# Optimization experiments

Hardware: AMD Instinct MI355X
Metric: run time of the kernel (lower is better)

Reference implementation:

```python
import jax, jax.numpy as jnp
import numpy as np

E = 32  # embedding_dim
B = 1048576

def setup_inputs() -> dict:
    key = jax.random.key(0)
    ks = jax.random.split(key, 16)
    def p(k, shape, scale=0.1):
        return jax.random.normal(k, shape, dtype=jnp.float32) * scale
    return {
        'x': jax.random.normal(ks[0], (B, 2, 5), dtype=jnp.float32),
        'fc_emb_w': p(ks[1], (E, 5)), 'fc_emb_b': p(ks[2], (E,)),
        'in_proj_w': p(ks[3], (3 * E, E)), 'in_proj_b': p(ks[4], (3 * E,)),
        'out_proj_w': p(ks[5], (E, E)), 'out_proj_b': p(ks[6], (E,)),
        'w_ih': p(ks[7], (E, E)), 'b_ih': p(ks[8], (E,)),
        'w_hh': p(ks[9], (E, E)), 'b_hh': p(ks[10], (E,)),
        'fc_dec_w': p(ks[11], (5, E)), 'fc_dec_b': p(ks[12], (5,)),
        'out_w': p(ks[13], (3, 5)), 'out_b': p(ks[14], (3,)),
    }

def gelu(x):
    return jax.nn.gelu(x, approximate=False)  # torch nn.GELU default (erf)

def reference(x, fc_emb_w, fc_emb_b, in_proj_w, in_proj_b,
              out_proj_w, out_proj_b, w_ih, b_ih, w_hh, b_hh,
              fc_dec_w, fc_dec_b, out_w, out_b):
    # per-token embedding: [B,2,5] -> [B,2,E]
    e = gelu(jnp.einsum('bsi,ei->bse', x, fc_emb_w) + fc_emb_b)
    # single-head self-attention (seq_len=2)
    wq, wk, wv = jnp.split(in_proj_w, 3, axis=0)
    bq, bk, bv = jnp.split(in_proj_b, 3, axis=0)
    q = jnp.einsum('bsd,ed->bse', e, wq) + bq
    k = jnp.einsum('bsd,ed->bse', e, wk) + bk
    v = jnp.einsum('bsd,ed->bse', e, wv) + bv
    scores = jnp.einsum('bqd,bkd->bqk', q, k) / jnp.sqrt(jnp.float32(E))
    attn = jax.nn.softmax(scores, axis=-1)
    o = jnp.einsum('bqk,bkd->bqd', attn, v)
    o = jnp.einsum('bsd,ed->bse', o, out_proj_w) + out_proj_b
    # 2-step tanh RNN, h0 = 0; final hidden state only
    h1 = jnp.tanh(o[:, 0] @ w_ih.T + b_ih + b_hh)
    h2 = jnp.tanh(o[:, 1] @ w_ih.T + b_ih + h1 @ w_hh.T + b_hh)
    # decode
    d = gelu(h2 @ fc_dec_w.T + fc_dec_b)
    return d @ out_w.T + out_b  # [B,3]
```

## Files before the change

kernel.cpp:

```cpp
#include <hip/hip_runtime.h>
#include <math.h>

#define BT 256

typedef _Float16 half2v __attribute__((ext_vector_type(2)));
typedef __fp16   fp16x2 __attribute__((ext_vector_type(2)));
typedef _Float16 half8  __attribute__((ext_vector_type(8)));
typedef float    f32x16 __attribute__((ext_vector_type(16)));

union U4H8 { unsigned int u[4]; half8 h; };

__device__ __forceinline__ half2v u2h(unsigned int u){
  union { unsigned int u; half2v h; } c; c.u = u; return c.h;
}
__device__ __forceinline__ unsigned int h2u(half2v h){
  union { unsigned int u; half2v h; } c; c.h = h; return c.u;
}
__device__ __forceinline__ half2v pkrtz(float a, float b){
  union { fp16x2 f; half2v h; } c;
  c.f = __builtin_amdgcn_cvt_pkrtz(a, b);
  return c.h;
}
__device__ __forceinline__ float fdot2(half2v a, half2v b, float c){
  return __builtin_amdgcn_fdot2(a, b, c, false);
}
__device__ __forceinline__ float frcp(float x){ return __builtin_amdgcn_rcpf(x); }

__device__ __forceinline__ unsigned int pk_rne(float a, float b){
  half2v h; h.x = (_Float16)a; h.y = (_Float16)b; return h2u(h);
}

__device__ __forceinline__ float gelu_erf(float v){
  float z  = v * 0.70710678118654752f;
  float az = fabsf(z);
  float t  = frcp(fmaf(0.47047f, az, 1.0f));
  float poly = t*fmaf(t, fmaf(t, 0.7478556f, -0.0958798f), 0.3480242f);
  float ex = __expf(-az*az);
  float erfv = fmaf(-poly, ex, 1.0f);
  erfv = (z < 0.0f) ? -erfv : erfv;
  return 0.5f*v*(1.0f + erfv);
}
__device__ __forceinline__ float tanh_fast(float v){
  float t = __expf(2.0f*v);
  return 1.0f - 2.0f*frcp(t + 1.0f);
}

__device__ __forceinline__ half2v gelu_pk(half2v x){
  const _Float16 a0 = (_Float16)0.3989423f,  a1 = (_Float16)-0.0663157f,
                 a2 = (_Float16)0.0096298f,  a3 = (_Float16)-0.00095967f,
                 a4 = (_Float16)0.000048f,   hp = (_Float16)0.5f,
                 hn = (_Float16)-0.5f;
  const half2v A0={a0,a0}, A1={a1,a1}, A2={a2,a2}, A3={a3,a3}, A4={a4,a4};
  const half2v HP={hp,hp}, HN={hn,hn};
  half2v t = x*x;
  half2v q = A4*t + A3;
  q = q*t + A2;
  q = q*t + A1;
  q = q*t + A0;
  half2v u = x*q;
#if __has_builtin(__builtin_elementwise_min)
  u = __builtin_elementwise_max(u, HN);
  u = __builtin_elementwise_min(u, HP);
#else
  u.x = u.x > hp ? hp : (u.x < hn ? hn : u.x);
  u.y = u.y > hp ? hp : (u.y < hn ? hn : u.y);
#endif
  return x*(u + HP);
}

__global__ void prep_kernel(const float* __restrict__ inw, const float* __restrict__ inb,
                            const float* __restrict__ opw, const float* __restrict__ opb,
                            const float* __restrict__ wih, const float* __restrict__ bih,
                            const float* __restrict__ bhh, const float* __restrict__ whh,
                            const float* __restrict__ decw, const float* __restrict__ embw,
                            const float* __restrict__ decb,
                            unsigned int* __restrict__ wsu){
  __shared__ float sA[1024], sP[1024], sM[1024], sT[32], sWV[32], sBM[32];
  int tx = threadIdx.x & 31;
  int ty = threadIdx.x >> 5;
  float accA = 0.f, accP = 0.f;
  #pragma unroll
  for (int m = 0; m < 32; m++){
    accA += inw[m*32 + ty] * inw[1024 + m*32 + tx];
    accP += opw[ty*32 + m] * inw[2048 + m*32 + tx];
  }
  sA[ty*32 + tx] = accA;
  sP[ty*32 + tx] = accP;
  if (ty == 0){
    float aw = 0.f;
    #pragma unroll
    for (int m = 0; m < 32; m++) aw += inb[m] * inw[1024 + m*32 + tx];
    sWV[tx] = aw;
  }
  if (ty == 1){
    float at = opb[tx];
    #pragma unroll
    for (int m = 0; m < 32; m++) at += opw[tx*32 + m] * inb[64 + m];
    sT[tx] = at;
  }
  __syncthreads();
  float accM = 0.f;
  #pragma unroll
  for (int m = 0; m < 32; m++) accM += wih[ty*32 + m] * sP[m*32 + tx];
  sM[ty*32 + tx] = accM;
  if (ty == 2){
    float ab = bih[tx] + bhh[tx];
    #pragma unroll
    for (int m = 0; m < 32; m++) ab += wih[tx*32 + m] * sT[m];
    sBM[tx] = ab;
  }
  __syncthreads();
  int t = threadIdx.x;
  if (t < 512){
    int r = t >> 4, c2 = (t & 15)*2;
    wsu[t]        = pk_rne(sA[r*32+c2],  sA[r*32+c2+1]);
    wsu[512 + t]  = pk_rne(sM[r*32+c2],  sM[r*32+c2+1]);
    wsu[1024 + t] = pk_rne(whh[r*32+c2], whh[r*32+c2+1]);
    wsu[1536 + t] = (r < 5) ? pk_rne(decw[r*32+c2], decw[r*32+c2+1]) : 0u;
  } else {
    int q = t - 512;
    if (q < 256){
      int j = q >> 3, cc = (q & 7)*2;
      float a = (cc   < 5) ? embw[j*5+cc]   : 0.f;
      float b = (cc+1 < 5) ? embw[j*5+cc+1] : 0.f;
      wsu[2048 + q] = pk_rne(a, b);
    } else if (q < 272){
      int k = (q - 256)*2;
      wsu[2304 + (q-256)] = pk_rne(sWV[k], sWV[k+1]);
    } else if (q < 304){
      ((float*)wsu)[2320 + (q-272)] = sBM[q-272];
    } else if (q < 336){
      int i = q - 304;
      ((float*)wsu)[2352 + i] = (i < 5) ? decb[i] : 0.f;
    }
  }
}

__device__ __forceinline__ half8 ldfrag(const unsigned int* __restrict__ p){
  U4H8 t; t.u[0]=p[0]; t.u[1]=p[1]; t.u[2]=p[2]; t.u[3]=p[3]; return t.h;
}

struct BF { U4H8 b1, b2; };
__device__ __forceinline__ BF toB_pk(const unsigned int* pk, bool g){
  unsigned int s0 = g?pk[0]:pk[2], s1 = g?pk[1]:pk[3],
               s2 = g?pk[4]:pk[6], s3 = g?pk[5]:pk[7];
  unsigned int r0 = __shfl_xor(s0,32), r1 = __shfl_xor(s1,32);
  unsigned int r2 = __shfl_xor(s2,32), r3 = __shfl_xor(s3,32);
  BF o;
  o.b1.u[0]=g?r0:pk[0]; o.b1.u[1]=g?r1:pk[1]; o.b1.u[2]=g?pk[2]:r0; o.b1.u[3]=g?pk[3]:r1;
  o.b2.u[0]=g?r2:pk[4]; o.b2.u[1]=g?r3:pk[5]; o.b2.u[2]=g?pk[6]:r2; o.b2.u[3]=g?pk[7]:r3;
  return o;
}

__device__ __forceinline__ f32x16 ldbias(const float* __restrict__ p, int grp){
  const float4* b = (const float4*)(p + 4*grp);
  float4 q0 = b[0], q1 = b[2], q2 = b[4], q3 = b[6];
  f32x16 c;
  c[0]=q0.x; c[1]=q0.y; c[2]=q0.z; c[3]=q0.w;
  c[4]=q1.x; c[5]=q1.y; c[6]=q1.z; c[7]=q1.w;
  c[8]=q2.x; c[9]=q2.y; c[10]=q2.z; c[11]=q2.w;
  c[12]=q3.x; c[13]=q3.y; c[14]=q3.z; c[15]=q3.w;
  return c;
}

__global__ __launch_bounds__(BT) void fused_kernel(
    const float* __restrict__ x,
    const unsigned int* __restrict__ wsu,
    const float* __restrict__ embb,
    const float* __restrict__ outw, const float* __restrict__ outb,
    float* __restrict__ y, int B)
{
  int tid  = threadIdx.x;
  int lane = tid & 63;
  int col  = lane & 31;
  bool g   = (lane >> 5) != 0;
  int grp  = g ? 1 : 0;
  long long base = ((long long)blockIdx.x*(BT/64) + (tid>>6)) * 32;
  if (base >= B) return;
  long long elem = base + col;

  const unsigned int* pA = wsu;
  const unsigned int* pM = wsu + 512;
  const unsigned int* pW = wsu + 1024;
  const unsigned int* pD = wsu + 1536;
  const unsigned int* pE = wsu + 2048;
  const unsigned int* pwv = wsu + 2304;
  const float* bMf = (const float*)(wsu + 2320);
  const float* dbf = (const float*)(wsu + 2352);

  half8 embA = ldfrag(pE + col*8  + grp*4);
  half8 A1   = ldfrag(pA + col*16 + grp*4), A2 = ldfrag(pA + col*16 + 8 + grp*4);
  half8 M1   = ldfrag(pM + col*16 + grp*4), M2 = ldfrag(pM + col*16 + 8 + grp*4);
  half8 W1   = ldfrag(pW + col*16 + grp*4), W2 = ldfrag(pW + col*16 + 8 + grp*4);
  half8 D1   = ldfrag(pD + col*16 + grp*4), D2 = ldfrag(pD + col*16 + 8 + grp*4);
  half2v wv1[4], wv2[4];
  #pragma unroll
  for (int j = 0; j < 4; j++){ wv1[j] = u2h(pwv[4*grp+j]); wv2[j] = u2h(pwv[8+4*grp+j]); }

  f32x16 cb_emb = ldbias(embb, grp);
  f32x16 cb_bM  = ldbias(bMf,  grp);
  f32x16 cb_db  = ldbias(dbf,  grp);

  const float2* xp = (const float2*)(x + elem*10ll);
  float2 p0 = xp[0], p1 = xp[1], p2 = xp[2], p3 = xp[3], p4 = xp[4];
  U4H8 xb0, xb1;
  xb0.u[0] = g ? 0u : h2u(pkrtz(p0.x, p0.y));
  xb0.u[1] = g ? 0u : h2u(pkrtz(p1.x, p1.y));
  xb0.u[2] = g ? 0u : h2u(pkrtz(p2.x, 0.f));
  xb0.u[3] = 0u;
  xb1.u[0] = g ? 0u : h2u(pkrtz(p2.y, p3.x));
  xb1.u[1] = g ? 0u : h2u(pkrtz(p3.y, p4.x));
  xb1.u[2] = g ? 0u : h2u(pkrtz(p4.y, 0.f));
  xb1.u[3] = 0u;

  f32x16 e0D = __builtin_amdgcn_mfma_f32_32x32x16_f16(embA, xb0.h, cb_emb, 0,0,0);
  f32x16 e1D = __builtin_amdgcn_mfma_f32_32x32x16_f16(embA, xb1.h, cb_emb, 0,0,0);
  unsigned int epk[8], dlpk[8];
  #pragma unroll
  for (int i = 0; i < 8; i++){
    half2v e0h = gelu_pk(pkrtz(e0D[2*i], e0D[2*i+1]));
    half2v e1h = gelu_pk(pkrtz(e1D[2*i], e1D[2*i+1]));
    epk[i]  = h2u(e0h);
    dlpk[i] = h2u(e1h - e0h);
  }

  BF e0B = toB_pk(epk, g);
  BF dB  = toB_pk(dlpk, g);
  f32x16 z16;
  #pragma unroll
  for (int i = 0; i < 16; i++) z16[i] = 0.f;
  f32x16 gD = __builtin_amdgcn_mfma_f32_32x32x16_f16(A1, dB.b1.h, z16, 0,0,0);
  gD = __builtin_amdgcn_mfma_f32_32x32x16_f16(A2, dB.b2.h, gD, 0,0,0);

  float t0 = 0.f, t1 = 0.f, dw = 0.f;
  #pragma unroll
  for (int i = 0; i < 8; i++){
    half2v gp = pkrtz(gD[2*i], gD[2*i+1]);
    t0 = fdot2(u2h(epk[i]),  gp, t0);
    t1 = fdot2(u2h(dlpk[i]), gp, t1);
  }
  #pragma unroll
  for (int j = 0; j < 4; j++){
    dw = fdot2(wv1[j], u2h(dB.b1.u[j]), dw);
    dw = fdot2(wv2[j], u2h(dB.b2.u[j]), dw);
  }
  t0 += __shfl_xor(t0, 32);
  t1 += __shfl_xor(t1, 32);
  dw += __shfl_xor(dw, 32);

  const float iss = 0.17677669529663689f;
  float a01 = frcp(1.0f + __expf(-((t0      + dw)*iss)));
  float a11 = frcp(1.0f + __expf(-((t0 + t1 + dw)*iss)));

  _Float16 q01 = (_Float16)a01, qda = (_Float16)(a11 - a01);
  half8 v01 = {q01,q01,q01,q01,q01,q01,q01,q01};
  half8 vda = {qda,qda,qda,qda,qda,qda,qda,qda};
  half8 c0B1 = dB.b1.h*v01 + e0B.b1.h, c0B2 = dB.b2.h*v01 + e0B.b2.h;
  half8 c1B1 = dB.b1.h*vda + c0B1,     c1B2 = dB.b2.h*vda + c0B2;

  f32x16 h1D = __builtin_amdgcn_mfma_f32_32x32x16_f16(M1, c0B1, cb_bM, 0,0,0);
  h1D = __builtin_amdgcn_mfma_f32_32x32x16_f16(M2, c0B2, h1D, 0,0,0);
  unsigned int h1pk[8];
  #pragma unroll
  for (int i = 0; i < 8; i++)
    h1pk[i] = h2u(pkrtz(tanh_fast(h1D[2*i]), tanh_fast(h1D[2*i+1])));
  BF h1B = toB_pk(h1pk, g);

  f32x16 h2D = __builtin_amdgcn_mfma_f32_32x32x16_f16(M1, c1B1, cb_bM, 0,0,0);
  h2D = __builtin_amdgcn_mfma_f32_32x32x16_f16(M2, c1B2, h2D, 0,0,0);
  h2D = __builtin_amdgcn_mfma_f32_32x32x16_f16(W1, h1B.b1.h, h2D, 0,0,0);
  h2D = __builtin_amdgcn_mfma_f32_32x32x16_f16(W2, h1B.b2.h, h2D, 0,0,0);
  unsigned int h2pk[8];
  #pragma unroll
  for (int i = 0; i < 8; i++)
    h2pk[i] = h2u(pkrtz(tanh_fast(h2D[2*i]), tanh_fast(h2D[2*i+1])));
  BF h2B = toB_pk(h2pk, g);

  f32x16 dvD = __builtin_amdgcn_mfma_f32_32x32x16_f16(D1, h2B.b1.h, cb_db, 0,0,0);
  dvD = __builtin_amdgcn_mfma_f32_32x32x16_f16(D2, h2B.b2.h, dvD, 0,0,0);
  float dv4 = __shfl_xor(dvD[0], 32);

  float d0 = gelu_erf(dvD[0]), d1 = gelu_erf(dvD[1]), d2 = gelu_erf(dvD[2]),
        d3 = gelu_erf(dvD[3]), d4 = gelu_erf(dv4);
  float y0 = outb[0] + outw[0]*d0 + outw[1]*d1 + outw[2]*d2 + outw[3]*d3 + outw[4]*d4;
  float y1 = outb[1] + outw[5]*d0 + outw[6]*d1 + outw[7]*d2 + outw[8]*d3 + outw[9]*d4;
  float y2 = outb[2] + outw[10]*d0 + outw[11]*d1 + outw[12]*d2 + outw[13]*d3 + outw[14]*d4;
  if (lane < 32){
    float* yp = y + elem*3ll;
    yp[0] = y0; yp[1] = y1; yp[2] = y2;
  }
}

extern "C" void kernel_launch(void* const* d_in, const int* in_sizes, int n_in,
                              void* d_out, int out_size, void* d_ws, size_t ws_size,
                              hipStream_t stream){
  const float* x    = (const float*)d_in[0];
  const float* embw = (const float*)d_in[1];
  const float* embb = (const float*)d_in[2];
  const float* inw  = (const float*)d_in[3];
  const float* inb  = (const float*)d_in[4];
  const float* opw  = (const float*)d_in[5];
  const float* opb  = (const float*)d_in[6];
  const float* wih  = (const float*)d_in[7];
  const float* bih  = (const float*)d_in[8];
  const float* whh  = (const float*)d_in[9];
  const float* bhh  = (const float*)d_in[10];
  const float* decw = (const float*)d_in[11];
  const float* decb = (const float*)d_in[12];
  const float* outw = (const float*)d_in[13];
  const float* outb = (const float*)d_in[14];
  float* y = (float*)d_out;
  unsigned int* wsu = (unsigned int*)d_ws;

  int B = in_sizes[0] / 10;
  int elems_per_block = (BT/64)*32;

  prep_kernel<<<1, 1024, 0, stream>>>(inw, inb, opw, opb, wih, bih, bhh,
                                      whh, decw, embw, decb, wsu);
  fused_kernel<<<(B + elems_per_block - 1)/elems_per_block, BT, 0, stream>>>(
      x, wsu, embb, outw, outb, y, B);
}
```

Before: 155.6 us.

## Permute packed weight columns to drop cross-lane shuffles between MFMA stages

The prep kernel now writes the weight fragments in a permuted column order, so the MFMA D-layout outputs can be fed directly as B operands without the toB_pk shuffle exchanges. The attention value-bias vector is permuted to match. tanh moves from an exp-based form to a clamped Pade rational approximation. The decoder bias is added in scalar form after the MFMA instead of being loaded as a bias fragment. The intent is fewer cross-lane shuffles and fewer transcendental ops per element. The risk is a correctness error if the permutation does not match the MFMA layout, plus lower tanh accuracy near the clamp.

```diff
diff --git a/kernel.cpp b/kernel.cpp
--- a/kernel.cpp
+++ b/kernel.cpp
@@ -40,9 +40,13 @@
   erfv = (z < 0.0f) ? -erfv : erfv;
   return 0.5f*v*(1.0f + erfv);
 }
-__device__ __forceinline__ float tanh_fast(float v){
-  float t = __expf(2.0f*v);
-  return 1.0f - 2.0f*frcp(t + 1.0f);
+
+__device__ __forceinline__ float tanh_pade(float x){
+  x = fminf(3.0f, fmaxf(-3.0f, x));
+  float t = x*x;
+  float n = fmaf(t + 105.0f, t, 945.0f);
+  float d = fmaf(fmaf(15.0f, t, 420.0f), t, 945.0f);
+  return x*n*frcp(d);
 }
 
 __device__ __forceinline__ half2v gelu_pk(half2v x){
@@ -73,9 +77,8 @@
                             const float* __restrict__ wih, const float* __restrict__ bih,
                             const float* __restrict__ bhh, const float* __restrict__ whh,
                             const float* __restrict__ decw, const float* __restrict__ embw,
-                            const float* __restrict__ decb,
                             unsigned int* __restrict__ wsu){
-  __shared__ float sA[1024], sP[1024], sM[1024], sT[32], sWV[32], sBM[32];
+  __shared__ float sA[1024], sP[1024], sM[1024], sT[32], sWV[32];
   int tx = threadIdx.x & 31;
   int ty = threadIdx.x >> 5;
   float accA = 0.f, accP = 0.f;
@@ -107,49 +110,34 @@
     float ab = bih[tx] + bhh[tx];
     #pragma unroll
     for (int m = 0; m < 32; m++) ab += wih[tx*32 + m] * sT[m];
-    sBM[tx] = ab;
+    ((float*)wsu)[2320 + tx] = ab;
   }
   __syncthreads();
   int t = threadIdx.x;
   if (t < 512){
-    int r = t >> 4, c2 = (t & 15)*2;
-    wsu[t]        = pk_rne(sA[r*32+c2],  sA[r*32+c2+1]);
-    wsu[512 + t]  = pk_rne(sM[r*32+c2],  sM[r*32+c2+1]);
-    wsu[1024 + t] = pk_rne(whh[r*32+c2], whh[r*32+c2+1]);
-    wsu[1536 + t] = (r < 5) ? pk_rne(decw[r*32+c2], decw[r*32+c2+1]) : 0u;
-  } else {
-    int q = t - 512;
-    if (q < 256){
-      int j = q >> 3, cc = (q & 7)*2;
-      float a = (cc   < 5) ? embw[j*5+cc]   : 0.f;
-      float b = (cc+1 < 5) ? embw[j*5+cc+1] : 0.f;
-      wsu[2048 + q] = pk_rne(a, b);
-    } else if (q < 272){
-      int k = (q - 256)*2;
-      wsu[2304 + (q-256)] = pk_rne(sWV[k], sWV[k+1]);
-    } else if (q < 304){
-      ((float*)wsu)[2320 + (q-272)] = sBM[q-272];
-    } else if (q < 336){
-      int i = q - 304;
-      ((float*)wsu)[2352 + i] = (i < 5) ? decb[i] : 0.f;
-    }
+    int r = t >> 4, j = t & 15;
+    int c0 = 16*(j>>3) + 8*((j>>1)&1) + 4*((j>>2)&1) + 2*(j&1);
+    wsu[t]        = pk_rne(sA[r*32+c0],  sA[r*32+c0+1]);
+    wsu[512 + t]  = pk_rne(sM[r*32+c0],  sM[r*32+c0+1]);
+    wsu[1024 + t] = pk_rne(whh[r*32+c0], whh[r*32+c0+1]);
+    wsu[1536 + t] = (r < 5) ? pk_rne(decw[r*32+c0], decw[r*32+c0+1]) : 0u;
+  } else if (t < 768){
+    int q = t - 512, j2 = q >> 3, cc = (q & 7)*2;
+    float a = (cc   < 5) ? embw[j2*5+cc]   : 0.f;
+    float b = (cc+1 < 5) ? embw[j2*5+cc+1] : 0.f;
+    wsu[2048 + q] = pk_rne(a, b);
+  } else if (t < 784){
+    int q = t - 768, gg = q >> 3, j = q & 7;
+    int r0 = 2*(j&1) + 8*(j>>1) + 4*gg;
+    wsu[2304 + q] = pk_rne(sWV[r0], sWV[r0+1]);
   }
 }
 
 __device__ __forceinline__ half8 ldfrag(const unsigned int* __restrict__ p){
   U4H8 t; t.u[0]=p[0]; t.u[1]=p[1]; t.u[2]=p[2]; t.u[3]=p[3]; return t.h;
 }
-
-struct BF { U4H8 b1, b2; };
-__device__ __forceinline__ BF toB_pk(const unsigned int* pk, bool g){
-  unsigned int s0 = g?pk[0]:pk[2], s1 = g?pk[1]:pk[3],
-               s2 = g?pk[4]:pk[6], s3 = g?pk[5]:pk[7];
-  unsigned int r0 = __shfl_xor(s0,32), r1 = __shfl_xor(s1,32);
-  unsigned int r2 = __shfl_xor(s2,32), r3 = __shfl_xor(s3,32);
-  BF o;
-  o.b1.u[0]=g?r0:pk[0]; o.b1.u[1]=g?r1:pk[1]; o.b1.u[2]=g?pk[2]:r0; o.b1.u[3]=g?pk[3]:r1;
-  o.b2.u[0]=g?r2:pk[4]; o.b2.u[1]=g?r3:pk[5]; o.b2.u[2]=g?pk[6]:r2; o.b2.u[3]=g?pk[7]:r3;
-  return o;
+__device__ __forceinline__ half8 h8of(const unsigned int* q){
+  U4H8 t; t.u[0]=q[0]; t.u[1]=q[1]; t.u[2]=q[2]; t.u[3]=q[3]; return t.h;
 }
 
 __device__ __forceinline__ f32x16 ldbias(const float* __restrict__ p, int grp){
@@ -167,6 +155,7 @@
     const float* __restrict__ x,
     const unsigned int* __restrict__ wsu,
     const float* __restrict__ embb,
+    const float* __restrict__ decb,
     const float* __restrict__ outw, const float* __restrict__ outb,
     float* __restrict__ y, int B)
 {
@@ -186,20 +175,18 @@
   const unsigned int* pE = wsu + 2048;
   const unsigned int* pwv = wsu + 2304;
   const float* bMf = (const float*)(wsu + 2320);
-  const float* dbf = (const float*)(wsu + 2352);
 
   half8 embA = ldfrag(pE + col*8  + grp*4);
   half8 A1   = ldfrag(pA + col*16 + grp*4), A2 = ldfrag(pA + col*16 + 8 + grp*4);
   half8 M1   = ldfrag(pM + col*16 + grp*4), M2 = ldfrag(pM + col*16 + 8 + grp*4);
   half8 W1   = ldfrag(pW + col*16 + grp*4), W2 = ldfrag(pW + col*16 + 8 + grp*4);
   half8 D1   = ldfrag(pD + col*16 + grp*4), D2 = ldfrag(pD + col*16 + 8 + grp*4);
-  half2v wv1[4], wv2[4];
-  #pragma unroll
-  for (int j = 0; j < 4; j++){ wv1[j] = u2h(pwv[4*grp+j]); wv2[j] = u2h(pwv[8+4*grp+j]); }
+  half2v wv[8];
+  #pragma unroll
+  for (int j = 0; j < 8; j++) wv[j] = u2h(pwv[grp*8 + j]);
 
   f32x16 cb_emb = ldbias(embb, grp);
   f32x16 cb_bM  = ldbias(bMf,  grp);
-  f32x16 cb_db  = ldbias(dbf,  grp);
 
   const float2* xp = (const float2*)(x + elem*10ll);
   float2 p0 = xp[0], p1 = xp[1], p2 = xp[2], p3 = xp[3], p4 = xp[4];
@@ -224,13 +211,11 @@
     dlpk[i] = h2u(e1h - e0h);
   }
 
-  BF e0B = toB_pk(epk, g);
-  BF dB  = toB_pk(dlpk, g);
   f32x16 z16;
   #pragma unroll
   for (int i = 0; i < 16; i++) z16[i] = 0.f;
-  f32x16 gD = __builtin_amdgcn_mfma_f32_32x32x16_f16(A1, dB.b1.h, z16, 0,0,0);
-  gD = __builtin_amdgcn_mfma_f32_32x32x16_f16(A2, dB.b2.h, gD, 0,0,0);
+  f32x16 gD = __builtin_amdgcn_mfma_f32_32x32x16_f16(A1, h8of(dlpk), z16, 0,0,0);
+  gD = __builtin_amdgcn_mfma_f32_32x32x16_f16(A2, h8of(dlpk+4), gD, 0,0,0);
 
   float t0 = 0.f, t1 = 0.f, dw = 0.f;
   #pragma unroll
@@ -238,11 +223,7 @@
     half2v gp = pkrtz(gD[2*i], gD[2*i+1]);
     t0 = fdot2(u2h(epk[i]),  gp, t0);
     t1 = fdot2(u2h(dlpk[i]), gp, t1);
-  }
-  #pragma unroll
-  for (int j = 0; j < 4; j++){
-    dw = fdot2(wv1[j], u2h(dB.b1.u[j]), dw);
-    dw = fdot2(wv2[j], u2h(dB.b2.u[j]), dw);
+    dw = fdot2(wv[i], u2h(dlpk[i]), dw);
   }
   t0 += __shfl_xor(t0, 32);
   t1 += __shfl_xor(t1, 32);
@@ -253,35 +234,40 @@
   float a11 = frcp(1.0f + __expf(-((t0 + t1 + dw)*iss)));
 
   _Float16 q01 = (_Float16)a01, qda = (_Float16)(a11 - a01);
-  half8 v01 = {q01,q01,q01,q01,q01,q01,q01,q01};
-  half8 vda = {qda,qda,qda,qda,qda,qda,qda,qda};
-  half8 c0B1 = dB.b1.h*v01 + e0B.b1.h, c0B2 = dB.b2.h*v01 + e0B.b2.h;
-  half8 c1B1 = dB.b1.h*vda + c0B1,     c1B2 = dB.b2.h*vda + c0B2;
-
-  f32x16 h1D = __builtin_amdgcn_mfma_f32_32x32x16_f16(M1, c0B1, cb_bM, 0,0,0);
-  h1D = __builtin_amdgcn_mfma_f32_32x32x16_f16(M2, c0B2, h1D, 0,0,0);
+  half2v s01 = {q01,q01}, sda = {qda,qda};
+  unsigned int c0pk[8], c1pk[8];
+  #pragma unroll
+  for (int j = 0; j < 8; j++){
+    half2v c0 = u2h(dlpk[j])*s01 + u2h(epk[j]);
+    half2v c1 = u2h(dlpk[j])*sda + c0;
+    c0pk[j] = h2u(c0); c1pk[j] = h2u(c1);
+  }
+
+  f32x16 h1D = __builtin_amdgcn_mfma_f32_32x32x16_f16(M1, h8of(c0pk), cb_bM, 0,0,0);
+  h1D = __builtin_amdgcn_mfma_f32_32x32x16_f16(M2, h8of(c0pk+4), h1D, 0,0,0);
   unsigned int h1pk[8];
   #pragma unroll
   for (int i = 0; i < 8; i++)
-    h1pk[i] = h2u(pkrtz(tanh_fast(h1D[2*i]), tanh_fast(h1D[2*i+1])));
-  BF h1B = toB_pk(h1pk, g);
-
-  f32x16 h2D = __builtin_amdgcn_mfma_f32_32x32x16_f16(M1, c1B1, cb_bM, 0,0,0);
-  h2D = __builtin_amdgcn_mfma_f32_32x32x16_f16(M2, c1B2, h2D, 0,0,0);
-  h2D = __builtin_amdgcn_mfma_f32_32x32x16_f16(W1, h1B.b1.h, h2D, 0,0,0);
-  h2D = __builtin_amdgcn_mfma_f32_32x32x16_f16(W2, h1B.b2.h, h2D, 0,0,0);
+    h1pk[i] = h2u(pkrtz(tanh_pade(h1D[2*i]), tanh_pade(h1D[2*i+1])));
+
+  f32x16 h2D = __builtin_amdgcn_mfma_f32_32x32x16_f16(M1, h8of(c1pk), cb_bM, 0,0,0);
+  h2D = __builtin_amdgcn_mfma_f32_32x32x16_f16(M2, h8of(c1pk+4), h2D, 0,0,0);
+  h2D = __builtin_amdgcn_mfma_f32_32x32x16_f16(W1, h8of(h1pk),   h2D, 0,0,0);
+  h2D = __builtin_amdgcn_mfma_f32_32x32x16_f16(W2, h8of(h1pk+4), h2D, 0,0,0);
   unsigned int h2pk[8];
   #pragma unroll
   for (int i = 0; i < 8; i++)
-    h2pk[i] = h2u(pkrtz(tanh_fast(h2D[2*i]), tanh_fast(h2D[2*i+1])));
-  BF h2B = toB_pk(h2pk, g);
-
-  f32x16 dvD = __builtin_amdgcn_mfma_f32_32x32x16_f16(D1, h2B.b1.h, cb_db, 0,0,0);
-  dvD = __builtin_amdgcn_mfma_f32_32x32x16_f16(D2, h2B.b2.h, dvD, 0,0,0);
+    h2pk[i] = h2u(pkrtz(tanh_pade(h2D[2*i]), tanh_pade(h2D[2*i+1])));
+
+  f32x16 dvD = __builtin_amdgcn_mfma_f32_32x32x16_f16(D1, h8of(h2pk), z16, 0,0,0);
+  dvD = __builtin_amdgcn_mfma_f32_32x32x16_f16(D2, h8of(h2pk+4), dvD, 0,0,0);
   float dv4 = __shfl_xor(dvD[0], 32);
 
-  float d0 = gelu_erf(dvD[0]), d1 = gelu_erf(dvD[1]), d2 = gelu_erf(dvD[2]),
-        d3 = gelu_erf(dvD[3]), d4 = gelu_erf(dv4);
+  float d0 = gelu_erf(dvD[0] + decb[0]);
+  float d1 = gelu_erf(dvD[1] + decb[1]);
+  float d2 = gelu_erf(dvD[2] + decb[2]);
+  float d3 = gelu_erf(dvD[3] + decb[3]);
+  float d4 = gelu_erf(dv4    + decb[4]);
   float y0 = outb[0] + outw[0]*d0 + outw[1]*d1 + outw[2]*d2 + outw[3]*d3 + outw[4]*d4;
   float y1 = outb[1] + outw[5]*d0 + outw[6]*d1 + outw[7]*d2 + outw[8]*d3 + outw[9]*d4;
   float y2 = outb[2] + outw[10]*d0 + outw[11]*d1 + outw[12]*d2 + outw[13]*d3 + outw[14]*d4;
@@ -316,7 +302,7 @@
   int elems_per_block = (BT/64)*32;
 
   prep_kernel<<<1, 1024, 0, stream>>>(inw, inb, opw, opb, wih, bih, bhh,
-                                      whh, decw, embw, decb, wsu);
+                                      whh, decw, embw, wsu);
   fused_kernel<<<(B + elems_per_block - 1)/elems_per_block, BT, 0, stream>>>(
-      x, wsu, embb, outw, outb, y, B);
-}
+      x, wsu, embb, decb, outw, outb, y, B);
+}
```

Measured after the change: 158.0 us. Within noise of the previous version (+1.6%).
